# Performance work log

Hardware: AMD Instinct MI355X
Metric: run time of the kernel (lower is better)

Reference implementation:

```python
import jax, jax.numpy as jnp
import numpy as np

N_NODES = 50000


def setup_inputs() -> dict:
    key = jax.random.key(0)
    k1, k2, k3, k4, k5, k6 = jax.random.split(key, 6)
    features = jax.random.normal(k1, (N_NODES, 128), dtype=jnp.float32)
    anchor_distances = jax.random.uniform(k2, (N_NODES, 64), dtype=jnp.float32)
    W = jax.random.normal(k3, (192, 128), dtype=jnp.float32) * (1.0 / np.sqrt(192.0))
    b = jax.random.normal(k4, (128,), dtype=jnp.float32) * 0.01
    src = jax.random.randint(k5, (800000,), 0, N_NODES, dtype=jnp.int32)
    dst = jax.random.randint(k6, (800000,), 0, N_NODES, dtype=jnp.int32)
    return {"features": features, "anchor_distances": anchor_distances,
            "W": W, "b": b, "src": src, "dst": dst}


def reference(features, anchor_distances, W, b, src, dst):
    # Linear(in_feats + num_anchors -> hidden) + ReLU
    combined = jnp.concatenate([features, anchor_distances], axis=1)  # [N, 192]
    h = jax.nn.relu(combined @ W + b)                                  # [N, H]
    # copy_u + mean aggregation: mean of h[src] grouped by dst
    msg_sum = jax.ops.segment_sum(h[src], dst, num_segments=N_NODES)  # [N, H]
    deg = jax.ops.segment_sum(jnp.ones_like(dst, dtype=h.dtype), dst,
                              num_segments=N_NODES)                    # [N]
    # DGL mean leaves 0 for isolated nodes; divide by max(deg, 1)
    out = msg_sum / jnp.maximum(deg, 1.0)[:, None]
    return out
```

## Files before the change

### kernel.cpp

```cpp
#include <hip/hip_runtime.h>
#include <hip/hip_bf16.h>


#define N_NODES 50000
#define N_EDGES 800000
#define HID 128
#define FDIM 128
#define ADIM 64
#define KDIM 192

#define BKT_SH 5
#define BKT_NODES 32
#define NBUCKETS ((N_NODES + BKT_NODES - 1) / BKT_NODES)
#define CAP 1024
#define PC_NBLK 256
#define PC_CHUNK ((N_EDGES + PC_NBLK - 1) / PC_NBLK)
#define EPT 13
#define GEMM_NBLK ((N_NODES + 31) / 32)
#define SA_LD 200

typedef __attribute__((ext_vector_type(8))) short short8;
typedef __attribute__((ext_vector_type(4))) float f32x4;
typedef __attribute__((ext_vector_type(4))) unsigned int u32x4;

__device__ inline unsigned short f2bf(float f) {
  unsigned u = __float_as_uint(f);
  u += 0x7FFFu + ((u >> 16) & 1u);
  return (unsigned short)(u >> 16);
}
__device__ inline unsigned pk2bf(float a, float b) {
  return (unsigned)f2bf(a) | ((unsigned)f2bf(b) << 16);
}
__device__ inline float bf2f(unsigned short s) {
  return __uint_as_float(((unsigned)s) << 16);
}

__global__ __launch_bounds__(256) void wbt_kernel(
    const float* __restrict__ W, unsigned short* __restrict__ WbTf,
    int* __restrict__ bcur) {
  if (blockIdx.x == 0) {
    for (int i = threadIdx.x; i < NBUCKETS; i += 256) bcur[i] = 0;
  }
  int idx = blockIdx.x * 256 + threadIdx.x;
  if (idx >= 2 * 4 * 6 * 64 * 8) return;
  int j = idx & 7;
  int lane = (idx >> 3) & 63;
  int frag = idx >> 9;
  int kk = frag % 6, p = frag / 6;
  int wn = p >> 2, nt = p & 3;
  int col = wn * 64 + nt * 16 + (lane & 15);
  int k = kk * 32 + (lane >> 4) * 8 + j;
  WbTf[idx] = f2bf(W[k * HID + col]);
}

#define SMEM_BYTES (32 * SA_LD * 2)
__global__ __launch_bounds__(256) void gemm_pscatter_kernel(
    const float* __restrict__ F, const float* __restrict__ A,
    const unsigned short* __restrict__ WbTf, const float* __restrict__ bias,
    unsigned short* __restrict__ hb,
    const int* __restrict__ src, const int* __restrict__ dst,
    int* __restrict__ bcur, unsigned* __restrict__ edata, int nrows) {
  __shared__ __align__(16) char smem_raw[SMEM_BYTES];

  if (blockIdx.x < PC_NBLK) {
    int* lh = (int*)smem_raw;
    int* lc = lh + NBUCKETS;
    int bp = blockIdx.x;
    for (int i = threadIdx.x; i < NBUCKETS; i += 256) lh[i] = 0;
    __syncthreads();
    int base = bp * PC_CHUNK;
    int end = base + PC_CHUNK; if (end > N_EDGES) end = N_EDGES;
    int rd[EPT], rs[EPT];
#pragma unroll
    for (int k = 0; k < EPT; ++k) {
      int j = base + threadIdx.x + k * 256;
      if (j < end) {
        rd[k] = dst[j];
        rs[k] = src[j];
        atomicAdd(&lh[rd[k] >> BKT_SH], 1);
      } else {
        rd[k] = -1;
      }
    }
    __syncthreads();
    for (int i = threadIdx.x; i < NBUCKETS; i += 256) {
      int c = lh[i];
      lh[i] = c ? atomicAdd(&bcur[i], c) : 0;
      lc[i] = 0;
    }
    __syncthreads();
#pragma unroll
    for (int k = 0; k < EPT; ++k) {
      if (rd[k] >= 0) {
        int bk = rd[k] >> BKT_SH, dl = rd[k] & (BKT_NODES - 1);
        int p = lh[bk] + atomicAdd(&lc[bk], 1);
        if (p < CAP)
          edata[(bk << 10) + p] = (unsigned)rs[k] | ((unsigned)dl << 16);
      }
    }
    return;
  }

  unsigned short* sA = (unsigned short*)smem_raw;
  const int gblk = blockIdx.x - PC_NBLK;
  const int tid = threadIdx.x;
  const int lane = tid & 63;
  const int wave = tid >> 6;
  const int wm = wave >> 1, wn = wave & 1;
  const int l15 = lane & 15, lg = lane >> 4;
  const int blockrow = gblk * 32;

#pragma unroll
  for (int it = 0; it < 4; ++it) {
    int i = tid + it * 256;
    int row = i >> 5, c4 = (i & 31) * 4;
    int crow = blockrow + row; crow = crow < nrows ? crow : (nrows - 1);
    float4 v = *(const float4*)(F + (size_t)crow * FDIM + c4);
    *(uint2*)(sA + row * SA_LD + c4) = make_uint2(pk2bf(v.x, v.y), pk2bf(v.z, v.w));
  }
#pragma unroll
  for (int it = 0; it < 2; ++it) {
    int i = tid + it * 256;
    int row = i >> 4, c4 = (i & 15) * 4;
    int crow = blockrow + row; crow = crow < nrows ? crow : (nrows - 1);
    float4 v = *(const float4*)(A + (size_t)crow * ADIM + c4);
    *(uint2*)(sA + row * SA_LD + FDIM + c4) = make_uint2(pk2bf(v.x, v.y), pk2bf(v.z, v.w));
  }

  short8 Bf[24];
#pragma unroll
  for (int nt = 0; nt < 4; ++nt)
#pragma unroll
    for (int kk = 0; kk < 6; ++kk)
      Bf[nt * 6 + kk] = *(const short8*)(
          WbTf + ((((wn * 4 + nt) * 6 + kk) << 9) + (lane << 3)));

  __syncthreads();

  short8 Af[6];
  const int rowl = wm * 16 + l15;
#pragma unroll
  for (int kk = 0; kk < 6; ++kk)
    Af[kk] = *(const short8*)(sA + rowl * SA_LD + kk * 32 + lg * 8);

  f32x4 acc[4] = {{0,0,0,0},{0,0,0,0},{0,0,0,0},{0,0,0,0}};
#pragma unroll
  for (int nt = 0; nt < 4; ++nt)
#pragma unroll
    for (int kk = 0; kk < 6; ++kk)
      acc[nt] = __builtin_amdgcn_mfma_f32_16x16x32_bf16(
          Af[kk], Bf[nt * 6 + kk], acc[nt], 0, 0, 0);

  const int rowbase = blockrow + wm * 16;
#pragma unroll
  for (int nt = 0; nt < 4; ++nt) {
    int col = wn * 64 + nt * 16 + l15;
    float bv = bias[col];
#pragma unroll
    for (int q = 0; q < 4; ++q) {
      int row = rowbase + lg * 4 + q;
      if (row < nrows) {
        float v = fmaxf(acc[nt][q] + bv, 0.f);
        hb[(size_t)row * HID + col] = f2bf(v);
      }
    }
  }
}

__device__ inline int wave_incl_scan(int v, int lane) {
#pragma unroll
  for (int off = 1; off < 64; off <<= 1) {
    int t = __shfl_up(v, off, 64);
    if (lane >= off) v += t;
  }
  return v;
}

#define EPT_A (CAP / 256)
__global__ __launch_bounds__(256) void bucket_agg_kernel(
    const unsigned short* __restrict__ hb, const int* __restrict__ bcur,
    const unsigned* __restrict__ edata, float* __restrict__ out) {
  int b = blockIdx.x;
  int nbase = b << BKT_SH;
  int nloc = N_NODES - nbase; if (nloc > BKT_NODES) nloc = BKT_NODES;
  int gb = b << 10;
  int cnt = bcur[b]; cnt = cnt < CAP ? cnt : CAP;
  int t = threadIdx.x, lane = t & 63, wave = t >> 6;
  int g = lane >> 4, l16 = lane & 15;

  __shared__ unsigned short ss[CAP];
  __shared__ int loff[BKT_NODES + 1];
  __shared__ int lcnt[BKT_NODES];
  __shared__ int lcur[BKT_NODES];

  unsigned er[EPT_A];
  if (t < BKT_NODES) lcnt[t] = 0;
  __syncthreads();
#pragma unroll
  for (int k = 0; k < EPT_A; ++k) {
    int j = t + k * 256;
    if (j < cnt) {
      er[k] = edata[gb + j];
      atomicAdd(&lcnt[er[k] >> 16], 1);
    } else {
      er[k] = 0xFFFFFFFFu;
    }
  }
  __syncthreads();
  if (wave == 0) {
    int v = (lane < BKT_NODES) ? lcnt[lane] : 0;
    int incl = wave_incl_scan(v, lane);
    if (lane < BKT_NODES) {
      loff[lane + 1] = incl;
      lcur[lane] = incl - v;
    }
    if (lane == 0) loff[0] = 0;
  }
  __syncthreads();
#pragma unroll
  for (int k = 0; k < EPT_A; ++k) {
    if (er[k] != 0xFFFFFFFFu) {
      int p = atomicAdd(&lcur[er[k] >> 16], 1);
      ss[p] = (unsigned short)(er[k] & 0xFFFFu);
    }
  }
  __syncthreads();
  for (int n = wave; n < nloc; n += 4) {
    int s0 = loff[n], s1 = loff[n + 1];
    float acc[8] = {0, 0, 0, 0, 0, 0, 0, 0};
    int j = s0 + g;
    for (; j + 4 < s1; j += 8) {
      int e0 = ss[j], e1 = ss[j + 4];
      u32x4 v0 = *(const u32x4*)(hb + (size_t)e0 * HID + l16 * 8);
      u32x4 v1 = *(const u32x4*)(hb + (size_t)e1 * HID + l16 * 8);
#pragma unroll
      for (int i = 0; i < 4; ++i) {
        unsigned w0 = v0[i], w1 = v1[i];
        acc[2 * i]     += bf2f((unsigned short)(w0 & 0xFFFFu))
                        + bf2f((unsigned short)(w1 & 0xFFFFu));
        acc[2 * i + 1] += bf2f((unsigned short)(w0 >> 16))
                        + bf2f((unsigned short)(w1 >> 16));
      }
    }
    if (j < s1) {
      int e0 = ss[j];
      u32x4 v0 = *(const u32x4*)(hb + (size_t)e0 * HID + l16 * 8);
#pragma unroll
      for (int i = 0; i < 4; ++i) {
        unsigned w0 = v0[i];
        acc[2 * i]     += bf2f((unsigned short)(w0 & 0xFFFFu));
        acc[2 * i + 1] += bf2f((unsigned short)(w0 >> 16));
      }
    }
#pragma unroll
    for (int i = 0; i < 8; ++i) {
      acc[i] += __shfl_xor(acc[i], 16, 64);
      acc[i] += __shfl_xor(acc[i], 32, 64);
    }
    if (g == 0) {
      int d = s1 - s0;
      float inv = 1.0f / (float)(d > 1 ? d : 1);
      float* po = out + (size_t)(nbase + n) * HID + l16 * 8;
      *(float4*)po       = make_float4(acc[0]*inv, acc[1]*inv, acc[2]*inv, acc[3]*inv);
      *(float4*)(po + 4) = make_float4(acc[4]*inv, acc[5]*inv, acc[6]*inv, acc[7]*inv);
    }
  }
}

extern "C" void kernel_launch(void* const* d_in, const int* in_sizes, int n_in,
                              void* d_out, int out_size, void* d_ws, size_t ws_size,
                              hipStream_t stream) {
  const float* F   = (const float*)d_in[0];
  const float* A   = (const float*)d_in[1];
  const float* W   = (const float*)d_in[2];
  const float* b   = (const float*)d_in[3];
  const int*   src = (const int*)d_in[4];
  const int*   dst = (const int*)d_in[5];
  float* out = (float*)d_out;

  char* ws = (char*)d_ws;
  size_t off = 0;
  auto alloc = [&](size_t bytes) {
    char* p = ws + off;
    off += (bytes + 255) & ~(size_t)255;
    return p;
  };
  unsigned short* hb   = (unsigned short*)alloc((size_t)N_NODES * HID * 2);
  unsigned short* WbTf = (unsigned short*)alloc((size_t)HID * KDIM * 2);
  int* bcur = (int*)alloc((size_t)NBUCKETS * sizeof(int));
  unsigned* edata = (unsigned*)alloc((size_t)NBUCKETS * CAP * sizeof(unsigned));
  (void)ws_size;

  wbt_kernel<<<(KDIM * HID + 255) / 256, 256, 0, stream>>>(W, WbTf, bcur);
  gemm_pscatter_kernel<<<PC_NBLK + GEMM_NBLK, 256, 0, stream>>>(
      F, A, WbTf, b, hb, src, dst, bcur, edata, N_NODES);
  bucket_agg_kernel<<<NBUCKETS, 256, 0, stream>>>(hb, bcur, edata, out);
}
```

Measured before the change: 67.05 us.

## Split bucket aggregation into column slabs and use nontemporal edge loads and stores

```diff
diff --git a/kernel.cpp b/kernel.cpp
--- a/kernel.cpp
+++ b/kernel.cpp
@@ -21,6 +21,7 @@
 
 typedef __attribute__((ext_vector_type(8))) short short8;
 typedef __attribute__((ext_vector_type(4))) float f32x4;
+typedef __attribute__((ext_vector_type(2))) float f32x2;
 typedef __attribute__((ext_vector_type(4))) unsigned int u32x4;
 
 __device__ inline unsigned short f2bf(float f) {
@@ -177,6 +178,8 @@
 }
 
 #define EPT_A (CAP / 256)
+#define NSLAB 4
+#define SLAB_COLS (HID / NSLAB)
 __global__ __launch_bounds__(256) void bucket_agg_kernel(
     const unsigned short* __restrict__ hb, const int* __restrict__ bcur,
     const unsigned* __restrict__ edata, float* __restrict__ out) {
@@ -200,7 +203,7 @@
   for (int k = 0; k < EPT_A; ++k) {
     int j = t + k * 256;
     if (j < cnt) {
-      er[k] = edata[gb + j];
+      er[k] = __builtin_nontemporal_load(edata + gb + j);
       atomicAdd(&lcnt[er[k] >> 16], 1);
     } else {
       er[k] = 0xFFFFFFFFu;
@@ -225,44 +228,42 @@
     }
   }
   __syncthreads();
-  for (int n = wave; n < nloc; n += 4) {
-    int s0 = loff[n], s1 = loff[n + 1];
-    float acc[8] = {0, 0, 0, 0, 0, 0, 0, 0};
-    int j = s0 + g;
-    for (; j + 4 < s1; j += 8) {
-      int e0 = ss[j], e1 = ss[j + 4];
-      u32x4 v0 = *(const u32x4*)(hb + (size_t)e0 * HID + l16 * 8);
-      u32x4 v1 = *(const u32x4*)(hb + (size_t)e1 * HID + l16 * 8);
-#pragma unroll
-      for (int i = 0; i < 4; ++i) {
-        unsigned w0 = v0[i], w1 = v1[i];
-        acc[2 * i]     += bf2f((unsigned short)(w0 & 0xFFFFu))
-                        + bf2f((unsigned short)(w1 & 0xFFFFu));
-        acc[2 * i + 1] += bf2f((unsigned short)(w0 >> 16))
-                        + bf2f((unsigned short)(w1 >> 16));
-      }
-    }
-    if (j < s1) {
-      int e0 = ss[j];
-      u32x4 v0 = *(const u32x4*)(hb + (size_t)e0 * HID + l16 * 8);
-#pragma unroll
-      for (int i = 0; i < 4; ++i) {
-        unsigned w0 = v0[i];
-        acc[2 * i]     += bf2f((unsigned short)(w0 & 0xFFFFu));
-        acc[2 * i + 1] += bf2f((unsigned short)(w0 >> 16));
-      }
-    }
-#pragma unroll
-    for (int i = 0; i < 8; ++i) {
-      acc[i] += __shfl_xor(acc[i], 16, 64);
-      acc[i] += __shfl_xor(acc[i], 32, 64);
-    }
-    if (g == 0) {
-      int d = s1 - s0;
-      float inv = 1.0f / (float)(d > 1 ? d : 1);
-      float* po = out + (size_t)(nbase + n) * HID + l16 * 8;
-      *(float4*)po       = make_float4(acc[0]*inv, acc[1]*inv, acc[2]*inv, acc[3]*inv);
-      *(float4*)(po + 4) = make_float4(acc[4]*inv, acc[5]*inv, acc[6]*inv, acc[7]*inv);
+
+#pragma unroll 1
+  for (int s = 0; s < NSLAB; ++s) {
+    const unsigned short* hbs = hb + s * SLAB_COLS + l16 * 2;
+    for (int n = wave; n < nloc; n += 4) {
+      int s0 = loff[n], s1 = loff[n + 1];
+      float a0 = 0.f, a1 = 0.f;
+      int j = s0 + g;
+      for (; j + 12 < s1; j += 16) {
+        unsigned w0 = *(const unsigned*)(hbs + (size_t)ss[j] * HID);
+        unsigned w1 = *(const unsigned*)(hbs + (size_t)ss[j + 4] * HID);
+        unsigned w2 = *(const unsigned*)(hbs + (size_t)ss[j + 8] * HID);
+        unsigned w3 = *(const unsigned*)(hbs + (size_t)ss[j + 12] * HID);
+        a0 += (bf2f((unsigned short)(w0 & 0xFFFFu))
+             + bf2f((unsigned short)(w1 & 0xFFFFu)))
+            + (bf2f((unsigned short)(w2 & 0xFFFFu))
+             + bf2f((unsigned short)(w3 & 0xFFFFu)));
+        a1 += (bf2f((unsigned short)(w0 >> 16))
+             + bf2f((unsigned short)(w1 >> 16)))
+            + (bf2f((unsigned short)(w2 >> 16))
+             + bf2f((unsigned short)(w3 >> 16)));
+      }
+      for (; j < s1; j += 4) {
+        unsigned w0 = *(const unsigned*)(hbs + (size_t)ss[j] * HID);
+        a0 += bf2f((unsigned short)(w0 & 0xFFFFu));
+        a1 += bf2f((unsigned short)(w0 >> 16));
+      }
+      a0 += __shfl_xor(a0, 16, 64); a0 += __shfl_xor(a0, 32, 64);
+      a1 += __shfl_xor(a1, 16, 64); a1 += __shfl_xor(a1, 32, 64);
+      if (g == 0) {
+        int d = s1 - s0;
+        float inv = 1.0f / (float)(d > 1 ? d : 1);
+        f32x2 o = {a0 * inv, a1 * inv};
+        __builtin_nontemporal_store(
+            o, (f32x2*)(out + (size_t)(nbase + n) * HID + s * SLAB_COLS + l16 * 2));
+      }
     }
   }
 }
```

New measurement: 90.30 us. 34.7% more time.
